# Performance work log

Hardware: AMD Instinct MI355X
Metric: run time of the kernel (lower is better)

Reference implementation:

```python
import jax, jax.numpy as jnp
import numpy as np

NEG_SLOPE = 0.2
LN_EPS = 1e-5


def _layer_norm(x, w, b):
    mu = jnp.mean(x, axis=-1, keepdims=True)
    var = jnp.mean((x - mu) ** 2, axis=-1, keepdims=True)
    return (x - mu) / jnp.sqrt(var + LN_EPS) * w + b


def setup_inputs() -> dict:
    N, E, R, H, D, HID, FF = 50000, 800000, 8, 4, 32, 128, 512
    key = jax.random.key(0)
    ks = jax.random.split(key, 12)
    s_w = float(np.sqrt(2.0 / (HID + HID)))  # xavier-ish scale
    return {
        "x": jax.random.normal(ks[0], (N, HID), jnp.float32),
        "weight": jax.random.normal(ks[1], (R, HID, HID), jnp.float32) * s_w,
        "root_weight": jax.random.normal(ks[2], (HID, HID), jnp.float32) * s_w,
        "edge_emb_table": jax.random.normal(ks[3], (R, HID), jnp.float32) * 0.01,
        "att_src": jax.random.normal(ks[4], (1, H, D), jnp.float32) * 0.1,
        "att_dst": jax.random.normal(ks[5], (1, H, D), jnp.float32) * 0.1,
        "att_edge": jax.random.normal(ks[6], (1, H, D), jnp.float32) * 0.1,
        "bias": jnp.zeros((HID,), jnp.float32),
        "norm1_w": jnp.ones((HID,), jnp.float32),
        "norm1_b": jnp.zeros((HID,), jnp.float32),
        "norm2_w": jnp.ones((HID,), jnp.float32),
        "norm2_b": jnp.zeros((HID,), jnp.float32),
        "ffn_w1": jax.random.normal(ks[7], (HID, FF), jnp.float32) * float(np.sqrt(2.0 / (HID + FF))),
        "ffn_b1": jnp.zeros((FF,), jnp.float32),
        "ffn_w2": jax.random.normal(ks[8], (FF, HID), jnp.float32) * float(np.sqrt(2.0 / (HID + FF))),
        "ffn_b2": jnp.zeros((HID,), jnp.float32),
        "edge_index": jax.random.randint(ks[9], (2, E), 0, N, jnp.int32),
        "edge_type": jax.random.randint(ks[10], (E,), 0, R, jnp.int32),
    }


def _rgat_conv(h, edge_index, edge_type, weight, root_weight, edge_emb_table,
               att_src, att_dst, att_edge, bias):
    N = h.shape[0]
    R = weight.shape[0]
    H, D = att_src.shape[1], att_src.shape[2]
    # relation-wise projection: [R, N, H, D]
    x_r = jnp.einsum('ni,rio->rno', h, weight).reshape(R, N, H, D)
    src, dst = edge_index[0], edge_index[1]
    x_src = x_r[edge_type, src]            # [E, H, D]
    x_dst = x_r[edge_type, dst]            # [E, H, D]
    edge_emb = edge_emb_table[edge_type].reshape(-1, H, D)
    alpha = (x_src * att_src).sum(-1) + (x_dst * att_dst).sum(-1) + (edge_emb * att_edge).sum(-1)  # [E, H]
    alpha = jax.nn.leaky_relu(alpha, NEG_SLOPE)
    # segment softmax over destination nodes
    amax = jax.ops.segment_max(alpha, dst, num_segments=N)  # [N, H]
    amax = jnp.where(jnp.isfinite(amax), amax, 0.0)
    ex = jnp.exp(alpha - amax[dst])
    den = jax.ops.segment_sum(ex, dst, num_segments=N)
    alpha = ex / (den[dst] + 1e-16)
    # dropout is identity in eval mode
    msg = x_src * alpha[..., None]         # [E, H, D]
    out = jax.ops.segment_sum(msg, dst, num_segments=N).reshape(N, H * D)
    return out + h @ root_weight + bias


def reference(x, weight, root_weight, edge_emb_table, att_src, att_dst, att_edge,
              bias, norm1_w, norm1_b, norm2_w, norm2_b,
              ffn_w1, ffn_b1, ffn_w2, ffn_b2, edge_index, edge_type):
    h = _layer_norm(x, norm1_w, norm1_b)
    h = _rgat_conv(h, edge_index, edge_type, weight, root_weight, edge_emb_table,
                   att_src, att_dst, att_edge, bias)
    h = jax.nn.elu(h)
    x = x + h
    h = _layer_norm(x, norm2_w, norm2_b)
    h = jax.nn.gelu(h @ ffn_w1 + ffn_b1, approximate=False) @ ffn_w2 + ffn_b2
    return x + h
```

## Files before the change

### kernel.cpp

```cpp
#include <hip/hip_runtime.h>
#include <hip/hip_bf16.h>
#include <math.h>

#define HID 128
#define NH  4
#define HD  32
#define FFD 512
#define RR  8
#define SCAN_B 1024
#define NB_SH 6

typedef __attribute__((ext_vector_type(8))) short bf16x8;
typedef __attribute__((ext_vector_type(4))) float f32x4;
typedef unsigned short u16;
typedef unsigned long long u64;

static __device__ __forceinline__ float bf2f(u16 u) {
    union { unsigned int i; float f; } v; v.i = ((unsigned int)u) << 16; return v.f;
}
static __device__ __forceinline__ u16 f2bf(float f) {
    union { float f; unsigned int i; } v; v.f = f;
    unsigned int x = v.i;
    return (u16)((x + 0x7fffu + ((x >> 16) & 1u)) >> 16);
}

__global__ void zeroout_kernel(float* out, int n) {
    int i = blockIdx.x * 256 + threadIdx.x;
    if (i < n) out[i] = 0.f;
}

__global__ void init_kernel(float* acc, int* deg2, int* bcnt, int NN, int NBK, int zacc) {
    int i = blockIdx.x * 256 + threadIdx.x;
    if (zacc && i < NN * HID) acc[i] = 0.f;
    if (i < NN * RR) deg2[i] = 0;
    if (i < NBK * 16) bcnt[i] = 0;
}

__global__ void stats_kernel(const float* in, float* mu, float* rs, int NN) {
    int row = blockIdx.x * 4 + (threadIdx.x >> 6);
    int lane = threadIdx.x & 63;
    if (row >= NN) return;
    const float* p = in + (size_t)row * HID;
    float v0 = p[lane], v1 = p[lane + 64];
    float s = v0 + v1;
    #pragma unroll
    for (int o = 32; o > 0; o >>= 1) s += __shfl_xor(s, o, 64);
    float m = s * (1.0f / HID);
    float d0 = v0 - m, d1 = v1 - m;
    float q = d0 * d0 + d1 * d1;
    #pragma unroll
    for (int o = 32; o > 0; o >>= 1) q += __shfl_xor(q, o, 64);
    if (lane == 0) { mu[row] = m; rs[row] = rsqrtf(q * (1.0f / HID) + 1e-5f); }
}

__global__ void hnorm_kernel(const float* in, const float* mu, const float* rs,
                             const float* lw, const float* lb, u16* out, int NN) {
    int idx = blockIdx.x * 256 + threadIdx.x;
    if (idx >= NN * (HID / 8)) return;
    int row = idx >> 4;
    int k0 = (idx & 15) * 8;
    float m = mu[row], r = rs[row];
    const float* p = in + (size_t)row * HID + k0;
    float4 a0 = *(const float4*)p, a1 = *(const float4*)(p + 4);
    float4 w0 = *(const float4*)(lw + k0), w1 = *(const float4*)(lw + k0 + 4);
    float4 b0 = *(const float4*)(lb + k0), b1 = *(const float4*)(lb + k0 + 4);
    bf16x8 o;
    o[0] = (short)f2bf((a0.x - m) * r * w0.x + b0.x);
    o[1] = (short)f2bf((a0.y - m) * r * w0.y + b0.y);
    o[2] = (short)f2bf((a0.z - m) * r * w0.z + b0.z);
    o[3] = (short)f2bf((a0.w - m) * r * w0.w + b0.w);
    o[4] = (short)f2bf((a1.x - m) * r * w1.x + b1.x);
    o[5] = (short)f2bf((a1.y - m) * r * w1.y + b1.y);
    o[6] = (short)f2bf((a1.z - m) * r * w1.z + b1.z);
    o[7] = (short)f2bf((a1.w - m) * r * w1.w + b1.w);
    *(bf16x8*)(out + (size_t)row * HID + k0) = o;
}

__global__ void transpose_kernel(const float* w, const float* rootw,
                                 const float* w1, const float* w2,
                                 u16* WT, u16* rootT, u16* W1T, u16* W2T, int R) {
    int i = blockIdx.x * 256 + threadIdx.x;
    int nW = R * HID * HID;
    if (i < nW) {
        int r = i / (HID * HID); int rem = i % (HID * HID);
        int n = rem / HID, k = rem % HID;
        WT[i] = f2bf(w[r * HID * HID + k * HID + n]);
    } else if (i < nW + HID * HID) {
        int j = i - nW; int n = j / HID, k = j % HID;
        rootT[j] = f2bf(rootw[k * HID + n]);
    } else if (i < nW + HID * HID + FFD * HID) {
        int j = i - nW - HID * HID; int n = j / HID, k = j % HID;
        W1T[j] = f2bf(w1[k * FFD + n]);
    } else if (i < nW + HID * HID + FFD * HID + HID * FFD) {
        int j = i - nW - HID * HID - FFD * HID; int n = j / FFD, k = j % FFD;
        W2T[j] = f2bf(w2[k * HID + n]);
    }
}

__global__ void vsd_kernel(const float* w, const float* att_src, const float* att_dst,
                           u16* Vsd, int R) {
    int idx = blockIdx.x * 256 + threadIdx.x;
    if (idx >= 64 * HID) return;
    int np = idx >> 7, k = idx & 127;
    int isDst = np >> 5, rh = np & 31, r = rh >> 2, h = rh & 3;
    const float* av = (isDst ? att_dst : att_src) + h * HD;
    const float* wp = w + (size_t)r * HID * HID + (size_t)k * HID + h * HD;
    float s = 0.f;
    #pragma unroll
    for (int d = 0; d < HD; d++) s += wp[d] * av[d];
    Vsd[idx] = f2bf(s);
}

__global__ void ae_kernel(const float* emb, const float* att_edge, float* ae, int R) {
    int i = threadIdx.x;
    if (i >= R * NH) return;
    int r = i >> 2, h = i & 3;
    float s = 0.f;
    #pragma unroll
    for (int d = 0; d < HD; d++)
        s += emb[r * HID + h * HD + d] * att_edge[h * HD + d];
    ae[i] = s;
}

template <int EPI, int TILED>
__global__ __launch_bounds__(256)
void gemmy_kernel(const u16* Araw, const u16* BT, u16* Cout, const float* bias,
                  int M, int N, int aOff, int cOff, int ytiles) {
    int w = threadIdx.x >> 6, lane = threadIdx.x & 63;
    int l15 = lane & 15, quad = lane >> 4;
    int m0 = blockIdx.x * 64 + w * 16;
    int rowA = m0 + l15; if (rowA > M - 1) rowA = M - 1;
    const u16* ap = Araw + (size_t)(aOff + rowA) * HID + quad * 8;
    bf16x8 a[4];
    #pragma unroll
    for (int kk = 0; kk < 4; kk++) a[kk] = *(const bf16x8*)(ap + kk * 32);

    __shared__ u16 tile[64][72];
    int rl2 = threadIdx.x >> 3, seg = threadIdx.x & 7;
    int ybase = blockIdx.y * ytiles;
    int nsub = N >> 6;
    for (int yi = 0; yi < ytiles; yi++) {
        int n0 = (ybase + yi) * 64;
        f32x4 accr[4] = {};
        #pragma unroll
        for (int kk = 0; kk < 4; kk++) {
            #pragma unroll
            for (int t = 0; t < 4; t++) {
                const u16* bp = BT + (size_t)(n0 + t * 16 + l15) * HID + quad * 8 + kk * 32;
                bf16x8 bfrag = *(const bf16x8*)bp;
                accr[t] = __builtin_amdgcn_mfma_f32_16x16x32_bf16(a[kk], bfrag, accr[t], 0, 0, 0);
            }
        }
        if (yi > 0) __syncthreads();
        #pragma unroll
        for (int t = 0; t < 4; t++) {
            int col = n0 + t * 16 + l15;
            #pragma unroll
            for (int j = 0; j < 4; j++) {
                float v = accr[t][j];
                if constexpr (EPI == 2) {
                    v += bias[col];
                    v = 0.5f * v * (1.0f + erff(v * 0.70710678118654752f));
                }
                tile[w * 16 + quad * 4 + j][t * 16 + l15] = f2bf(v);
            }
        }
        __syncthreads();
        if constexpr (TILED) {
            u16* tb = Cout + (((size_t)blockIdx.x * nsub + (ybase + yi)) << 12);
            #pragma unroll
            for (int h = 0; h < 2; h++) {
                int rl = h * 32 + rl2;
                int row = blockIdx.x * 64 + rl;
                if (row < M) {
                    *(bf16x8*)(tb + (rl << 6) + seg * 8) =
                        *(const bf16x8*)&tile[rl][seg * 8];
                }
            }
        } else {
            #pragma unroll
            for (int h = 0; h < 2; h++) {
                int rl = h * 32 + rl2;
                int row = blockIdx.x * 64 + rl;
                if (row < M) {
                    u16* dst = Cout + (size_t)(cOff + row) * N + n0 + seg * 8;
                    *(bf16x8*)dst = *(const bf16x8*)&tile[rl][seg * 8];
                }
            }
        }
    }
}

template <int AM, int EPI>
__global__ __launch_bounds__(256)
void gemm_kernel(const void* Araw, const float* mu, const float* rs,
                 const float* lw, const float* lb,
                 const u16* BT, void* Cout, const float* bias,
                 const float* acc, const float* xin, const float* invden,
                 int M, int N, int K, int aOff, int cOff) {
    int w = threadIdx.x >> 6, lane = threadIdx.x & 63;
    int l15 = lane & 15, quad = lane >> 4;
    int m0 = blockIdx.x * 64 + w * 16;
    int n0 = blockIdx.y * 64;
    int rowA = m0 + l15; if (rowA > M - 1) rowA = M - 1;
    int gA = aOff + rowA;
    float muv = 0.f, rsv = 0.f;
    if (AM != 2) { muv = mu[gA]; rsv = rs[gA]; }

    f32x4 accr[4] = {};
    for (int kc = 0; kc < K; kc += 32) {
        bf16x8 a;
        if (AM == 0) {
            const float* ap = (const float*)Araw + (size_t)gA * K + quad * 8 + kc;
            float4 xa0 = *(const float4*)(ap);
            float4 xa1 = *(const float4*)(ap + 4);
            float4 w0 = *(const float4*)(lw + kc + quad * 8);
            float4 w1v = *(const float4*)(lw + kc + quad * 8 + 4);
            float4 b0 = *(const float4*)(lb + kc + quad * 8);
            float4 b1v = *(const float4*)(lb + kc + quad * 8 + 4);
            a[0] = (short)f2bf((xa0.x - muv) * rsv * w0.x + b0.x);
            a[1] = (short)f2bf((xa0.y - muv) * rsv * w0.y + b0.y);
            a[2] = (short)f2bf((xa0.z - muv) * rsv * w0.z + b0.z);
            a[3] = (short)f2bf((xa0.w - muv) * rsv * w0.w + b0.w);
            a[4] = (short)f2bf((xa1.x - muv) * rsv * w1v.x + b1v.x);
            a[5] = (short)f2bf((xa1.y - muv) * rsv * w1v.y + b1v.y);
            a[6] = (short)f2bf((xa1.z - muv) * rsv * w1v.z + b1v.z);
            a[7] = (short)f2bf((xa1.w - muv) * rsv * w1v.w + b1v.w);
        } else {
            const u16* ap = (const u16*)Araw + (size_t)gA * K + quad * 8 + kc;
            a = *(const bf16x8*)ap;
        }
        #pragma unroll
        for (int t = 0; t < 4; t++) {
            const u16* bp = BT + (size_t)(n0 + t * 16 + l15) * K + quad * 8 + kc;
            bf16x8 bfrag = *(const bf16x8*)bp;
            accr[t] = __builtin_amdgcn_mfma_f32_16x16x32_bf16(a, bfrag, accr[t], 0, 0, 0);
        }
    }

    if constexpr (EPI == 0 || EPI == 2) {
        __shared__ u16 tile[64][72];
        #pragma unroll
        for (int t = 0; t < 4; t++) {
            int col = n0 + t * 16 + l15;
            #pragma unroll
            for (int j = 0; j < 4; j++) {
                float v = accr[t][j];
                if (EPI == 2) {
                    v += bias[col];
                    v = 0.5f * v * (1.0f + erff(v * 0.70710678118654752f));
                }
                tile[w * 16 + quad * 4 + j][t * 16 + l15] = f2bf(v);
            }
        }
        __syncthreads();
        int rl2 = threadIdx.x >> 3, seg = threadIdx.x & 7;
        #pragma unroll
        for (int h = 0; h < 2; h++) {
            int rl = h * 32 + rl2;
            int row = blockIdx.x * 64 + rl;
            if (row < M) {
                u16* dst = (u16*)Cout + (size_t)(cOff + row) * N + n0 + seg * 8;
                *(bf16x8*)dst = *(const bf16x8*)&tile[rl][seg * 8];
            }
        }
    } else {
        #pragma unroll
        for (int t = 0; t < 4; t++) {
            int col = n0 + t * 16 + l15;
            #pragma unroll
            for (int j = 0; j < 4; j++) {
                int row = m0 + quad * 4 + j;
                if (row < M) {
                    float v = accr[t][j];
                    int grow = cOff + row;
                    size_t off = (size_t)grow * N + col;
                    if (EPI == 1) {
                        float msg = acc[(size_t)grow * HID + col]
                                  * invden[(size_t)grow * NH + (col >> 5)];
                        float o = v + msg + bias[col];
                        o = o > 0.f ? o : expm1f(o);
                        ((float*)Cout)[off] = xin[off] + o;
                    } else if (EPI == 3) {
                        ((float*)Cout)[off] = v + bias[col] + xin[off];
                    } else if (EPI == 5) {
                        float* tab = (float*)Cout;
                        if (col < 32) tab[(size_t)grow * 32 + col] = v;
                        else tab[(size_t)(M + grow) * 32 + (col - 32)] = v;
                    }
                }
            }
        }
    }
}

__global__ void deg_kernel(const int* ei, const int* et, int* deg2, int E, int NN) {
    int e = blockIdx.x * 256 + threadIdx.x;
    if (e >= E) return;
    int s = ei[e], d = ei[E + e], r = et[e];
    if ((unsigned)d < (unsigned)NN && (unsigned)r < (unsigned)RR &&
        (unsigned)s < (unsigned)NN)
        atomicAdd(&deg2[d * RR + r], 1);
}

__global__ void scan1_kernel(const int* in, int* out, int* bsum, int n) {
    __shared__ int buf[SCAN_B];
    int i = blockIdx.x * SCAN_B + threadIdx.x;
    int v = (i < n) ? in[i] : 0;
    buf[threadIdx.x] = v;
    __syncthreads();
    for (int s = 1; s < SCAN_B; s <<= 1) {
        int t = (threadIdx.x >= s) ? buf[threadIdx.x - s] : 0;
        __syncthreads();
        buf[threadIdx.x] += t;
        __syncthreads();
    }
    if (i < n) out[i] = buf[threadIdx.x] - v;
    if (threadIdx.x == SCAN_B - 1) bsum[blockIdx.x] = buf[SCAN_B - 1];
}

__global__ void scan2_kernel(int* bsum, int nb) {
    __shared__ int buf[SCAN_B];
    int v = (threadIdx.x < nb) ? bsum[threadIdx.x] : 0;
    buf[threadIdx.x] = v;
    __syncthreads();
    for (int s = 1; s < SCAN_B; s <<= 1) {
        int t = (threadIdx.x >= s) ? buf[threadIdx.x - s] : 0;
        __syncthreads();
        buf[threadIdx.x] += t;
        __syncthreads();
    }
    if (threadIdx.x < nb) bsum[threadIdx.x] = buf[threadIdx.x] - v;
    if (threadIdx.x == SCAN_B - 1) bsum[nb] = buf[SCAN_B - 1];
}

__global__ void scan3_kernel(int* out, int* curpos, const int* bsum, int n, int nb) {
    int i = blockIdx.x * SCAN_B + threadIdx.x;
    if (i < n) {
        int o = out[i] + bsum[blockIdx.x];
        out[i] = o; curpos[i] = o;
    }
    if (i == 0) out[n] = bsum[nb];
}

__global__ void fillA_kernel(const int* ei, const int* et, const int* offs2,
                             int* bcnt, u64* tmp, int E, int NN) {
    int e = blockIdx.x * 256 + threadIdx.x;
    if (e >= E) return;
    int s = ei[e], d = ei[E + e], r = et[e];
    if ((unsigned)d >= (unsigned)NN || (unsigned)r >= (unsigned)RR ||
        (unsigned)s >= (unsigned)NN) return;
    int b = d >> NB_SH;
    int base = offs2[(b << NB_SH) * RR];
    int pos = atomicAdd(&bcnt[b * 16], 1);
    tmp[base + pos] = ((u64)d << 32) | (unsigned)((r << 24) | s);
}

__global__ void fillB_kernel(const u64* tmp, const int* offs2,
                             int* curpos2, int* rs_arr, int NN) {
    int b = blockIdx.x;
    int n0 = b << NB_SH;
    int n1 = n0 + (1 << NB_SH); if (n1 > NN) n1 = NN;
    int base = offs2[n0 * RR];
    int end  = offs2[n1 * RR];
    for (int i = base + threadIdx.x; i < end; i += 256) {
        u64 t = tmp[i];
        int d = (int)(t >> 32);
        unsigned v = (unsigned)t;
        int r = v >> 24;
        int pos = atomicAdd(&curpos2[d * RR + r], 1);
        rs_arr[pos] = (int)v;
    }
}

__global__ void wgt_kernel(const int* offs2, const int* rs_arr,
                           const float* asad, const float* ae,
                           float* wgt, float* invden, int NN, int E) {
    int n = blockIdx.x * 4 + (threadIdx.x >> 6);
    if (n >= NN) return;
    int lane = threadIdx.x & 63;
    int el = lane >> 2, h = lane & 3;
    int p0 = offs2[n * RR], p1 = offs2[n * RR + RR];
    const float* ad = asad + (size_t)NN * 32;
    float base[RR];
    #pragma unroll
    for (int r = 0; r < RR; r++)
        base[r] = ad[(size_t)n * 32 + r * 4 + h] + ae[r * 4 + h];
    float mx = -1e30f;
    for (int p = p0 + el; p < p1; p += 16) {
        unsigned v = (unsigned)rs_arr[p];
        int r = v >> 24, s = v & 0xFFFFFF;
        float a = asad[(size_t)s * 32 + r * 4 + h] + base[r];
        a = a > 0.f ? a : 0.2f * a;
        wgt[(size_t)p * NH + h] = a;
        mx = fmaxf(mx, a);
    }
    #pragma unroll
    for (int o = 4; o < 64; o <<= 1) mx = fmaxf(mx, __shfl_xor(mx, o, 64));
    float den = 0.f;
    for (int p = p0 + el; p < p1; p += 16) {
        float ex = __expf(wgt[(size_t)p * NH + h] - mx);
        wgt[(size_t)p * NH + h] = ex;
        den += ex;
    }
    #pragma unroll
    for (int o = 4; o < 64; o <<= 1) den += __shfl_xor(den, o, 64);
    if (el == 0) invden[n * NH + h] = 1.0f / (den + 1e-16f);
}

__global__ __launch_bounds__(256)
void msg1_kernel(const int* offs2, const int* rs_arr, const float* wgt,
                 const u16* xp, float* acc, int NN) {
    int n = blockIdx.x * 4 + (threadIdx.x >> 6);
    if (n >= NN) return;
    int lane = threadIdx.x & 63;
    int half = lane >> 5;
    int co = (lane & 31) << 1;
    int h = lane >> 4;
    int p0 = offs2[n * RR], p1 = offs2[n * RR + RR];
    float a0 = 0.f, a1 = 0.f;
    int p = p0;
    for (; p + 4 <= p1; p += 4) {
        unsigned v0 = (unsigned)rs_arr[p + 0];
        unsigned v1 = (unsigned)rs_arr[p + 1];
        unsigned v2 = (unsigned)rs_arr[p + 2];
        unsigned v3 = (unsigned)rs_arr[p + 3];
        unsigned s0 = v0 & 0xFFFFFFu, s1 = v1 & 0xFFFFFFu;
        unsigned s2 = v2 & 0xFFFFFFu, s3 = v3 & 0xFFFFFFu;
        unsigned z0 = *(const unsigned*)(xp
            + (((size_t)(s0 >> 6) * 16 + ((v0 >> 24) << 1) + half) << 12)
            + ((s0 & 63) << 6) + co);
        unsigned z1 = *(const unsigned*)(xp
            + (((size_t)(s1 >> 6) * 16 + ((v1 >> 24) << 1) + half) << 12)
            + ((s1 & 63) << 6) + co);
        unsigned z2 = *(const unsigned*)(xp
            + (((size_t)(s2 >> 6) * 16 + ((v2 >> 24) << 1) + half) << 12)
            + ((s2 & 63) << 6) + co);
        unsigned z3 = *(const unsigned*)(xp
            + (((size_t)(s3 >> 6) * 16 + ((v3 >> 24) << 1) + half) << 12)
            + ((s3 & 63) << 6) + co);
        float w0 = wgt[(size_t)(p + 0) * NH + h];
        float w1 = wgt[(size_t)(p + 1) * NH + h];
        float w2 = wgt[(size_t)(p + 2) * NH + h];
        float w3 = wgt[(size_t)(p + 3) * NH + h];
        a0 += w0 * bf2f((u16)z0) + w1 * bf2f((u16)z1)
            + w2 * bf2f((u16)z2) + w3 * bf2f((u16)z3);
        a1 += w0 * bf2f((u16)(z0 >> 16)) + w1 * bf2f((u16)(z1 >> 16))
            + w2 * bf2f((u16)(z2 >> 16)) + w3 * bf2f((u16)(z3 >> 16));
    }
    for (; p < p1; p++) {
        unsigned v = (unsigned)rs_arr[p];
        unsigned s = v & 0xFFFFFFu;
        unsigned z = *(const unsigned*)(xp
            + (((size_t)(s >> 6) * 16 + ((v >> 24) << 1) + half) << 12)
            + ((s & 63) << 6) + co);
        float wv = wgt[(size_t)p * NH + h];
        a0 += wv * bf2f((u16)z);
        a1 += wv * bf2f((u16)(z >> 16));
    }
    float2 o; o.x = a0; o.y = a1;
    *(float2*)(acc + (size_t)n * HID + (lane << 1)) = o;
}

__global__ void msg2_kernel(const int* offs2, const int* rs_arr, const float* wgt,
                            const u16* xp, float* acc, int rc, int nrel, int ldx,
                            int NN, int E) {
    int n = blockIdx.x;
    int c = threadIdx.x, h = c >> 5;
    int p0 = offs2[n * RR + rc], p1 = offs2[n * RR + rc + nrel];
    if (p0 >= p1) return;
    float av = acc[(size_t)n * HID + c];
    for (int p = p0; p < p1; p++) {
        unsigned v = (unsigned)rs_arr[p];
        int r = (v >> 24) - rc;
        int s = v & 0xFFFFFF;
        av += wgt[(size_t)p * NH + h] * bf2f(xp[(size_t)s * ldx + r * HID + c]);
    }
    acc[(size_t)n * HID + c] = av;
}

extern "C" void kernel_launch(void* const* d_in, const int* in_sizes, int n_in,
                              void* d_out, int out_size, void* d_ws, size_t ws_size,
                              hipStream_t stream) {
    const float* x        = (const float*)d_in[0];
    const float* w        = (const float*)d_in[1];
    const float* rootw    = (const float*)d_in[2];
    const float* emb      = (const float*)d_in[3];
    const float* att_src  = (const float*)d_in[4];
    const float* att_dst  = (const float*)d_in[5];
    const float* att_edge = (const float*)d_in[6];
    const float* bias     = (const float*)d_in[7];
    const float* n1w      = (const float*)d_in[8];
    const float* n1b      = (const float*)d_in[9];
    const float* n2w      = (const float*)d_in[10];
    const float* n2b      = (const float*)d_in[11];
    const float* w1       = (const float*)d_in[12];
    const float* b1       = (const float*)d_in[13];
    const float* w2       = (const float*)d_in[14];
    const float* b2       = (const float*)d_in[15];
    const int* ei = (const int*)d_in[16];
    const int* et = (const int*)d_in[17];

    int NN = in_sizes[0] / HID;
    int R  = in_sizes[1] / (HID * HID);
    int E  = in_sizes[17];
    int NR = NN * RR;
    int NBK = (NN + (1 << NB_SH) - 1) >> NB_SH;
    int gxN = (NN + 63) / 64;
    int Mpad = gxN * 64;

    char* p = (char*)d_ws;
    auto alloc = [&](size_t bytes) -> char* {
        char* q = p; p += (bytes + 255) & ~(size_t)255; return q;
    };
    int* offs2   = (int*)alloc((size_t)(NR + 1) * 4);
    int* rs_arr  = (int*)alloc((size_t)E * 4);
    u16* WTw   = (u16*)alloc((size_t)R * HID * HID * 2);
    u16* rootT = (u16*)alloc((size_t)HID * HID * 2);
    u16* W1T   = (u16*)alloc((size_t)FFD * HID * 2);
    u16* W2T   = (u16*)alloc((size_t)HID * FFD * 2);
    u16* Vsd   = (u16*)alloc((size_t)64 * HID * 2);
    float* ae  = (float*)alloc((size_t)R * NH * 4);
    float* mu1 = (float*)alloc((size_t)NN * 4);
    float* rs1 = (float*)alloc((size_t)NN * 4);
    float* mu2 = (float*)alloc((size_t)NN * 4);
    float* rs2 = (float*)alloc((size_t)NN * 4);
    float* asad   = (float*)alloc((size_t)NN * 64 * 4);
    float* invden = (float*)alloc((size_t)NN * NH * 4);
    float* wgt    = (float*)alloc((size_t)E * NH * 4);
    float* acc    = (float*)alloc((size_t)NN * HID * 4);

    int nbScan = (NR + SCAN_B - 1) / SCAN_B;
    int* deg2    = (int*)wgt;
    int* curpos2 = deg2 + NR;
    int* bsum    = curpos2 + NR;
    int* bcnt    = bsum + nbScan + 1;
    u64* tmp     = (u64*)(((size_t)(bcnt + NBK * 16) + 7) & ~(size_t)7);

    size_t usedFixed = (size_t)(p - (char*)d_ws);
    int nrel = 1;
    for (int t = 8; t > 1; t >>= 1) {
        size_t rows = (t == 8) ? (size_t)Mpad : (size_t)NN;
        if (ws_size >= usedFixed + rows * HID * t * 2 + 256) { nrel = t; break; }
    }
    size_t xrows = (nrel == 8) ? (size_t)Mpad : (size_t)NN;
    u16* xp = (u16*)alloc(xrows * HID * nrel * 2);
    u16* u_ch = xp;
    u16* hbuf = (u16*)asad;
    float* x2 = (float*)d_out;

    size_t used = (size_t)(p - (char*)d_ws);
    if (used > ws_size) {
        zeroout_kernel<<<(out_size + 255) / 256, 256, 0, stream>>>((float*)d_out, out_size);
        return;
    }

    int single = (nrel == RR) ? 1 : 0;
    int initN = single ? (NR > NBK * 16 ? NR : NBK * 16) : NN * HID;
    init_kernel<<<(initN + 255) / 256, 256, 0, stream>>>(acc, deg2, bcnt, NN, NBK,
                                                         single ? 0 : 1);
    stats_kernel<<<(NN + 3) / 4, 256, 0, stream>>>(x, mu1, rs1, NN);
    int nT = R * HID * HID + HID * HID + FFD * HID + HID * FFD;
    transpose_kernel<<<(nT + 255) / 256, 256, 0, stream>>>(w, rootw, w1, w2,
                                                           WTw, rootT, W1T, W2T, R);
    vsd_kernel<<<(64 * HID + 255) / 256, 256, 0, stream>>>(w, att_src, att_dst, Vsd, R);
    ae_kernel<<<1, 64, 0, stream>>>(emb, att_edge, ae, R);
    deg_kernel<<<(E + 255) / 256, 256, 0, stream>>>(ei, et, deg2, E, NN);
    scan1_kernel<<<nbScan, SCAN_B, 0, stream>>>(deg2, offs2, bsum, NR);
    scan2_kernel<<<1, SCAN_B, 0, stream>>>(bsum, nbScan);
    scan3_kernel<<<nbScan, SCAN_B, 0, stream>>>(offs2, curpos2, bsum, NR, nbScan);
    fillA_kernel<<<(E + 255) / 256, 256, 0, stream>>>(ei, et, offs2, bcnt, tmp, E, NN);
    fillB_kernel<<<NBK, 256, 0, stream>>>(tmp, offs2, curpos2, rs_arr, NN);

    gemm_kernel<0, 5><<<dim3(gxN, 1), 256, 0, stream>>>(
        x, mu1, rs1, n1w, n1b, Vsd, asad,
        nullptr, nullptr, nullptr, nullptr, NN, 64, HID, 0, 0);

    wgt_kernel<<<(NN + 3) / 4, 256, 0, stream>>>(
        offs2, rs_arr, asad, ae, wgt, invden, NN, E);

    hnorm_kernel<<<(NN * (HID / 8) + 255) / 256, 256, 0, stream>>>(
        x, mu1, rs1, n1w, n1b, hbuf, NN);

    if (single) {
        gemmy_kernel<0, 1><<<dim3(gxN, 2), 256, 0, stream>>>(
            hbuf, WTw, xp, nullptr, NN, HID * RR, 0, 0, 8);
        msg1_kernel<<<(NN + 3) / 4, 256, 0, stream>>>(offs2, rs_arr, wgt, xp, acc, NN);
    } else {
        for (int rc = 0; rc < RR; rc += nrel) {
            gemm_kernel<2, 0><<<dim3(gxN, (HID * nrel) / 64), 256, 0, stream>>>(
                hbuf, nullptr, nullptr, nullptr, nullptr, WTw + (size_t)rc * HID * HID,
                xp, nullptr, nullptr, nullptr, nullptr, NN, HID * nrel, HID, 0, 0);
            msg2_kernel<<<NN, HID, 0, stream>>>(offs2, rs_arr, wgt, xp, acc,
                                                rc, nrel, HID * nrel, NN, E);
        }
    }

    gemm_kernel<2, 1><<<dim3(gxN, HID / 64), 256, 0, stream>>>(
        hbuf, nullptr, nullptr, nullptr, nullptr, rootT, x2, bias, acc, x, invden,
        NN, HID, HID, 0, 0);

    stats_kernel<<<(NN + 3) / 4, 256, 0, stream>>>(x2, mu2, rs2, NN);
    hnorm_kernel<<<(NN * (HID / 8) + 255) / 256, 256, 0, stream>>>(
        x2, mu2, rs2, n2w, n2b, hbuf, NN);
    int nchunk = (nrel >= 4) ? 1 : (nrel == 2 ? 2 : 4);
    int NCH = (NN + nchunk - 1) / nchunk;
    for (int j = 0; j < nchunk; j++) {
        int r0 = j * NCH;
        int Mc = NN - r0; if (Mc > NCH) Mc = NCH;
        if (Mc <= 0) continue;
        int gxc = (Mc + 63) / 64;
        gemmy_kernel<2, 0><<<dim3(gxc, 2), 256, 0, stream>>>(
            hbuf, W1T, u_ch, b1, Mc, FFD, r0, 0, 4);
        gemm_kernel<2, 3><<<dim3(gxc, HID / 64), 256, 0, stream>>>(
            u_ch, nullptr, nullptr, nullptr, nullptr, W2T, (float*)d_out, b2,
            nullptr, x2, nullptr, Mc, HID, FFD, 0, r0);
    }
}
```

Before: 614.4 us.

## Merge independent prep stages into horizontally fused kernels with separate hbuf

Adds a workspace mode that gives the normalized activations their own buffer, so stages that used to be serialized can share one launch. fused1 combines the attention-score GEMM, the LayerNorm-to-bf16 pass and the edge bucketing fill in a single grid split by block index. fused2 combines the relation projection GEMM, written through an LDS tile into a tiled layout, with the softmax weight computation. The aim is to cut launch count and let independent work overlap on the GPU. In exchange it needs extra workspace and adds code paths, and blocks of very different cost now share one grid.

```diff
diff --git a/kernel.cpp b/kernel.cpp
--- a/kernel.cpp
+++ b/kernel.cpp
@@ -53,9 +53,9 @@
     if (lane == 0) { mu[row] = m; rs[row] = rsqrtf(q * (1.0f / HID) + 1e-5f); }
 }
 
-__global__ void hnorm_kernel(const float* in, const float* mu, const float* rs,
-                             const float* lw, const float* lb, u16* out, int NN) {
-    int idx = blockIdx.x * 256 + threadIdx.x;
+static __device__ __forceinline__
+void hnorm_body(int idx, const float* in, const float* mu, const float* rs,
+                const float* lw, const float* lb, u16* out, int NN) {
     if (idx >= NN * (HID / 8)) return;
     int row = idx >> 4;
     int k0 = (idx & 15) * 8;
@@ -74,6 +74,11 @@
     o[6] = (short)f2bf((a1.z - m) * r * w1.z + b1.z);
     o[7] = (short)f2bf((a1.w - m) * r * w1.w + b1.w);
     *(bf16x8*)(out + (size_t)row * HID + k0) = o;
+}
+
+__global__ void hnorm_kernel(const float* in, const float* mu, const float* rs,
+                             const float* lw, const float* lb, u16* out, int NN) {
+    hnorm_body(blockIdx.x * 256 + threadIdx.x, in, mu, rs, lw, lb, out, NN);
 }
 
 __global__ void transpose_kernel(const float* w, const float* rootw,
@@ -343,9 +348,9 @@
     if (i == 0) out[n] = bsum[nb];
 }
 
-__global__ void fillA_kernel(const int* ei, const int* et, const int* offs2,
-                             int* bcnt, u64* tmp, int E, int NN) {
-    int e = blockIdx.x * 256 + threadIdx.x;
+static __device__ __forceinline__
+void fillA_body(int e, const int* ei, const int* et, const int* offs2,
+                int* bcnt, u64* tmp, int E, int NN) {
     if (e >= E) return;
     int s = ei[e], d = ei[E + e], r = et[e];
     if ((unsigned)d >= (unsigned)NN || (unsigned)r >= (unsigned)RR ||
@@ -354,6 +359,11 @@
     int base = offs2[(b << NB_SH) * RR];
     int pos = atomicAdd(&bcnt[b * 16], 1);
     tmp[base + pos] = ((u64)d << 32) | (unsigned)((r << 24) | s);
+}
+
+__global__ void fillA_kernel(const int* ei, const int* et, const int* offs2,
+                             int* bcnt, u64* tmp, int E, int NN) {
+    fillA_body(blockIdx.x * 256 + threadIdx.x, ei, et, offs2, bcnt, tmp, E, NN);
 }
 
 __global__ void fillB_kernel(const u64* tmp, const int* offs2,
@@ -373,10 +383,10 @@
     }
 }
 
-__global__ void wgt_kernel(const int* offs2, const int* rs_arr,
-                           const float* asad, const float* ae,
-                           float* wgt, float* invden, int NN, int E) {
-    int n = blockIdx.x * 4 + (threadIdx.x >> 6);
+static __device__ __forceinline__
+void wgt_body(int n, const int* offs2, const int* rs_arr,
+              const float* asad, const float* ae,
+              float* wgtb, float* invden, int NN) {
     if (n >= NN) return;
     int lane = threadIdx.x & 63;
     int el = lane >> 2, h = lane & 3;
@@ -392,20 +402,143 @@
         int r = v >> 24, s = v & 0xFFFFFF;
         float a = asad[(size_t)s * 32 + r * 4 + h] + base[r];
         a = a > 0.f ? a : 0.2f * a;
-        wgt[(size_t)p * NH + h] = a;
+        wgtb[(size_t)p * NH + h] = a;
         mx = fmaxf(mx, a);
     }
     #pragma unroll
     for (int o = 4; o < 64; o <<= 1) mx = fmaxf(mx, __shfl_xor(mx, o, 64));
     float den = 0.f;
     for (int p = p0 + el; p < p1; p += 16) {
-        float ex = __expf(wgt[(size_t)p * NH + h] - mx);
-        wgt[(size_t)p * NH + h] = ex;
+        float ex = __expf(wgtb[(size_t)p * NH + h] - mx);
+        wgtb[(size_t)p * NH + h] = ex;
         den += ex;
     }
     #pragma unroll
     for (int o = 4; o < 64; o <<= 1) den += __shfl_xor(den, o, 64);
     if (el == 0) invden[n * NH + h] = 1.0f / (den + 1e-16f);
+}
+
+__global__ void wgt_kernel(const int* offs2, const int* rs_arr,
+                           const float* asad, const float* ae,
+                           float* wgtb, float* invden, int NN, int E) {
+    wgt_body(blockIdx.x * 4 + (threadIdx.x >> 6), offs2, rs_arr, asad, ae,
+             wgtb, invden, NN);
+}
+
+__global__ __launch_bounds__(256)
+void fused1_kernel(const float* x, const float* mu, const float* rs,
+                   const float* lw, const float* lb, const u16* Vsd, float* asad,
+                   u16* hb,
+                   const int* ei, const int* et, const int* offs2,
+                   int* bcnt, u64* tmp, int E, int NN, int gxN, int hB) {
+    int bid = blockIdx.x;
+    if (bid < gxN) {
+        int w = threadIdx.x >> 6, lane = threadIdx.x & 63;
+        int l15 = lane & 15, quad = lane >> 4;
+        int m0 = bid * 64 + w * 16;
+        int rowA = m0 + l15; if (rowA > NN - 1) rowA = NN - 1;
+        float muv = mu[rowA], rsv = rs[rowA];
+        f32x4 accr[4] = {};
+        for (int kc = 0; kc < HID; kc += 32) {
+            const float* ap = x + (size_t)rowA * HID + quad * 8 + kc;
+            float4 xa0 = *(const float4*)(ap);
+            float4 xa1 = *(const float4*)(ap + 4);
+            float4 w0 = *(const float4*)(lw + kc + quad * 8);
+            float4 w1v = *(const float4*)(lw + kc + quad * 8 + 4);
+            float4 b0 = *(const float4*)(lb + kc + quad * 8);
+            float4 b1v = *(const float4*)(lb + kc + quad * 8 + 4);
+            bf16x8 a;
+            a[0] = (short)f2bf((xa0.x - muv) * rsv * w0.x + b0.x);
+            a[1] = (short)f2bf((xa0.y - muv) * rsv * w0.y + b0.y);
+            a[2] = (short)f2bf((xa0.z - muv) * rsv * w0.z + b0.z);
+            a[3] = (short)f2bf((xa0.w - muv) * rsv * w0.w + b0.w);
+            a[4] = (short)f2bf((xa1.x - muv) * rsv * w1v.x + b1v.x);
+            a[5] = (short)f2bf((xa1.y - muv) * rsv * w1v.y + b1v.y);
+            a[6] = (short)f2bf((xa1.z - muv) * rsv * w1v.z + b1v.z);
+            a[7] = (short)f2bf((xa1.w - muv) * rsv * w1v.w + b1v.w);
+            #pragma unroll
+            for (int t = 0; t < 4; t++) {
+                const u16* bp = Vsd + (size_t)(t * 16 + l15) * HID + quad * 8 + kc;
+                bf16x8 bfrag = *(const bf16x8*)bp;
+                accr[t] = __builtin_amdgcn_mfma_f32_16x16x32_bf16(a, bfrag, accr[t], 0, 0, 0);
+            }
+        }
+        #pragma unroll
+        for (int t = 0; t < 4; t++) {
+            int col = t * 16 + l15;
+            #pragma unroll
+            for (int j = 0; j < 4; j++) {
+                int row = m0 + quad * 4 + j;
+                if (row < NN) {
+                    float v = accr[t][j];
+                    if (col < 32) asad[(size_t)row * 32 + col] = v;
+                    else asad[(size_t)(NN + row) * 32 + (col - 32)] = v;
+                }
+            }
+        }
+    } else if (bid < gxN + hB) {
+        hnorm_body((bid - gxN) * 256 + threadIdx.x, x, mu, rs, lw, lb, hb, NN);
+    } else {
+        fillA_body((bid - gxN - hB) * 256 + threadIdx.x, ei, et, offs2,
+                   bcnt, tmp, E, NN);
+    }
+}
+
+__global__ __launch_bounds__(256)
+void fused2_kernel(const u16* hb, const u16* WTw, u16* xp,
+                   const int* offs2, const int* rs_arr, const float* asad,
+                   const float* ae, float* wgtb, float* invden,
+                   int NN, int gxN, int projB) {
+    __shared__ u16 tile[64][72];
+    int bid = blockIdx.x;
+    if (bid < projB) {
+        int xb = bid % gxN, yb = bid / gxN;
+        int w = threadIdx.x >> 6, lane = threadIdx.x & 63;
+        int l15 = lane & 15, quad = lane >> 4;
+        int m0 = xb * 64 + w * 16;
+        int rowA = m0 + l15; if (rowA > NN - 1) rowA = NN - 1;
+        const u16* ap = hb + (size_t)rowA * HID + quad * 8;
+        bf16x8 a[4];
+        #pragma unroll
+        for (int kk = 0; kk < 4; kk++) a[kk] = *(const bf16x8*)(ap + kk * 32);
+        int rl2 = threadIdx.x >> 3, seg = threadIdx.x & 7;
+        int ybase = yb * 8;
+        for (int yi = 0; yi < 8; yi++) {
+            int n0 = (ybase + yi) * 64;
+            f32x4 accr[4] = {};
+            #pragma unroll
+            for (int kk = 0; kk < 4; kk++) {
+                #pragma unroll
+                for (int t = 0; t < 4; t++) {
+                    const u16* bp = WTw + (size_t)(n0 + t * 16 + l15) * HID + quad * 8 + kk * 32;
+                    bf16x8 bfrag = *(const bf16x8*)bp;
+                    accr[t] = __builtin_amdgcn_mfma_f32_16x16x32_bf16(a[kk], bfrag, accr[t], 0, 0, 0);
+                }
+            }
+            if (yi > 0) __syncthreads();
+            #pragma unroll
+            for (int t = 0; t < 4; t++) {
+                #pragma unroll
+                for (int j = 0; j < 4; j++) {
+                    tile[w * 16 + quad * 4 + j][t * 16 + l15] = f2bf(accr[t][j]);
+                }
+            }
+            __syncthreads();
+            u16* tb = xp + (((size_t)xb * 16 + (ybase + yi)) << 12);
+            #pragma unroll
+            for (int h = 0; h < 2; h++) {
+                int rl = h * 32 + rl2;
+                int row = xb * 64 + rl;
+                if (row < NN) {
+                    *(bf16x8*)(tb + (rl << 6) + seg * 8) =
+                        *(const bf16x8*)&tile[rl][seg * 8];
+                }
+            }
+        }
+    } else {
+        wgt_body((bid - projB) * 4 + (threadIdx.x >> 6), offs2, rs_arr,
+                 asad, ae, wgtb, invden, NN);
+    }
 }
 
 __global__ __launch_bounds__(256)
@@ -538,15 +671,28 @@
     u64* tmp     = (u64*)(((size_t)(bcnt + NBK * 16) + 7) & ~(size_t)7);
 
     size_t usedFixed = (size_t)(p - (char*)d_ws);
-    int nrel = 1;
-    for (int t = 8; t > 1; t >>= 1) {
-        size_t rows = (t == 8) ? (size_t)Mpad : (size_t)NN;
-        if (ws_size >= usedFixed + rows * HID * t * 2 + 256) { nrel = t; break; }
-    }
-    size_t xrows = (nrel == 8) ? (size_t)Mpad : (size_t)NN;
-    u16* xp = (u16*)alloc(xrows * HID * nrel * 2);
+    size_t xpTiled = (size_t)Mpad * HID * RR * 2;
+    size_t hbufSz  = (size_t)NN * HID * 2;
+    int mode; int nrel = RR;
+    u16 *xp, *hbuf;
+    if (ws_size >= usedFixed + hbufSz + xpTiled + 512) {
+        mode = 2;
+        hbuf = (u16*)alloc(hbufSz);
+        xp = (u16*)alloc(xpTiled);
+    } else if (ws_size >= usedFixed + xpTiled + 256) {
+        mode = 1;
+        hbuf = (u16*)asad;
+        xp = (u16*)alloc(xpTiled);
+    } else {
+        mode = 0;
+        nrel = 1;
+        for (int t = 4; t > 1; t >>= 1) {
+            if (ws_size >= usedFixed + (size_t)NN * HID * t * 2 + 256) { nrel = t; break; }
+        }
+        hbuf = (u16*)asad;
+        xp = (u16*)alloc((size_t)NN * HID * nrel * 2);
+    }
     u16* u_ch = xp;
-    u16* hbuf = (u16*)asad;
     float* x2 = (float*)d_out;
 
     size_t used = (size_t)(p - (char*)d_ws);
@@ -555,10 +701,9 @@
         return;
     }
 
-    int single = (nrel == RR) ? 1 : 0;
-    int initN = single ? (NR > NBK * 16 ? NR : NBK * 16) : NN * HID;
+    int initN = (mode != 0) ? (NR > NBK * 16 ? NR : NBK * 16) : NN * HID;
     init_kernel<<<(initN + 255) / 256, 256, 0, stream>>>(acc, deg2, bcnt, NN, NBK,
-                                                         single ? 0 : 1);
+                                                         mode == 0 ? 1 : 0);
     stats_kernel<<<(NN + 3) / 4, 256, 0, stream>>>(x, mu1, rs1, NN);
     int nT = R * HID * HID + HID * HID + FFD * HID + HID * FFD;
     transpose_kernel<<<(nT + 255) / 256, 256, 0, stream>>>(w, rootw, w1, w2,
@@ -569,30 +714,41 @@
     scan1_kernel<<<nbScan, SCAN_B, 0, stream>>>(deg2, offs2, bsum, NR);
     scan2_kernel<<<1, SCAN_B, 0, stream>>>(bsum, nbScan);
     scan3_kernel<<<nbScan, SCAN_B, 0, stream>>>(offs2, curpos2, bsum, NR, nbScan);
-    fillA_kernel<<<(E + 255) / 256, 256, 0, stream>>>(ei, et, offs2, bcnt, tmp, E, NN);
-    fillB_kernel<<<NBK, 256, 0, stream>>>(tmp, offs2, curpos2, rs_arr, NN);
-
-    gemm_kernel<0, 5><<<dim3(gxN, 1), 256, 0, stream>>>(
-        x, mu1, rs1, n1w, n1b, Vsd, asad,
-        nullptr, nullptr, nullptr, nullptr, NN, 64, HID, 0, 0);
-
-    wgt_kernel<<<(NN + 3) / 4, 256, 0, stream>>>(
-        offs2, rs_arr, asad, ae, wgt, invden, NN, E);
-
-    hnorm_kernel<<<(NN * (HID / 8) + 255) / 256, 256, 0, stream>>>(
-        x, mu1, rs1, n1w, n1b, hbuf, NN);
-
-    if (single) {
-        gemmy_kernel<0, 1><<<dim3(gxN, 2), 256, 0, stream>>>(
-            hbuf, WTw, xp, nullptr, NN, HID * RR, 0, 0, 8);
+
+    int hB = (NN * (HID / 8) + 255) / 256;
+    int fB = (E + 255) / 256;
+
+    if (mode == 2) {
+        fused1_kernel<<<gxN + hB + fB, 256, 0, stream>>>(
+            x, mu1, rs1, n1w, n1b, Vsd, asad, hbuf,
+            ei, et, offs2, bcnt, tmp, E, NN, gxN, hB);
+        fillB_kernel<<<NBK, 256, 0, stream>>>(tmp, offs2, curpos2, rs_arr, NN);
+        int projB = gxN * 2;
+        int wB = (NN + 3) / 4;
+        fused2_kernel<<<projB + wB, 256, 0, stream>>>(
+            hbuf, WTw, xp, offs2, rs_arr, asad, ae, wgt, invden, NN, gxN, projB);
         msg1_kernel<<<(NN + 3) / 4, 256, 0, stream>>>(offs2, rs_arr, wgt, xp, acc, NN);
     } else {
-        for (int rc = 0; rc < RR; rc += nrel) {
-            gemm_kernel<2, 0><<<dim3(gxN, (HID * nrel) / 64), 256, 0, stream>>>(
-                hbuf, nullptr, nullptr, nullptr, nullptr, WTw + (size_t)rc * HID * HID,
-                xp, nullptr, nullptr, nullptr, nullptr, NN, HID * nrel, HID, 0, 0);
-            msg2_kernel<<<NN, HID, 0, stream>>>(offs2, rs_arr, wgt, xp, acc,
-                                                rc, nrel, HID * nrel, NN, E);
+        fillA_kernel<<<fB, 256, 0, stream>>>(ei, et, offs2, bcnt, tmp, E, NN);
+        fillB_kernel<<<NBK, 256, 0, stream>>>(tmp, offs2, curpos2, rs_arr, NN);
+        gemm_kernel<0, 5><<<dim3(gxN, 1), 256, 0, stream>>>(
+            x, mu1, rs1, n1w, n1b, Vsd, asad,
+            nullptr, nullptr, nullptr, nullptr, NN, 64, HID, 0, 0);
+        wgt_kernel<<<(NN + 3) / 4, 256, 0, stream>>>(
+            offs2, rs_arr, asad, ae, wgt, invden, NN, E);
+        hnorm_kernel<<<hB, 256, 0, stream>>>(x, mu1, rs1, n1w, n1b, hbuf, NN);
+        if (mode == 1) {
+            gemmy_kernel<0, 1><<<dim3(gxN, 2), 256, 0, stream>>>(
+                hbuf, WTw, xp, nullptr, NN, HID * RR, 0, 0, 8);
+            msg1_kernel<<<(NN + 3) / 4, 256, 0, stream>>>(offs2, rs_arr, wgt, xp, acc, NN);
+        } else {
+            for (int rc = 0; rc < RR; rc += nrel) {
+                gemm_kernel<2, 0><<<dim3(gxN, (HID * nrel) / 64), 256, 0, stream>>>(
+                    hbuf, nullptr, nullptr, nullptr, nullptr, WTw + (size_t)rc * HID * HID,
+                    xp, nullptr, nullptr, nullptr, nullptr, NN, HID * nrel, HID, 0, 0);
+                msg2_kernel<<<NN, HID, 0, stream>>>(offs2, rs_arr, wgt, xp, acc,
+                                                    rc, nrel, HID * nrel, NN, E);
+            }
         }
     }
 
@@ -601,9 +757,8 @@
         NN, HID, HID, 0, 0);
 
     stats_kernel<<<(NN + 3) / 4, 256, 0, stream>>>(x2, mu2, rs2, NN);
-    hnorm_kernel<<<(NN * (HID / 8) + 255) / 256, 256, 0, stream>>>(
-        x2, mu2, rs2, n2w, n2b, hbuf, NN);
-    int nchunk = (nrel >= 4) ? 1 : (nrel == 2 ? 2 : 4);
+    hnorm_kernel<<<hB, 256, 0, stream>>>(x2, mu2, rs2, n2w, n2b, hbuf, NN);
+    int nchunk = (mode != 0) ? 1 : (nrel >= 4 ? 1 : (nrel == 2 ? 2 : 4));
     int NCH = (NN + nchunk - 1) / nchunk;
     for (int j = 0; j < nchunk; j++) {
         int r0 = j * NCH;
```

After: 588.1 us. -4.3%, faster.
